# Kernel optimization log

Measured on AMD Instinct MI355X. Metric: run time of the kernel, lower is better.

## Reference

```python
import jax, jax.numpy as jnp
import numpy as np

H = 1024
NH = 16
DH = H // NH
I = 4096
EPS = 1e-6


def _rms(x, g):
    # RMSNorm: x * rsqrt(mean(x^2, -1) + eps) * g
    return x * jax.lax.rsqrt(jnp.mean(x * x, axis=-1, keepdims=True) + EPS) * g


def _squash(v):
    # norm^2/(1+norm^2)/norm * v == norm/(1+norm^2) * v
    n = jnp.sqrt(jnp.sum(v * v, axis=-1, keepdims=True))
    return v * n / (1.0 + n * n)


def setup_inputs() -> dict:
    key = jax.random.key(0)
    ks = jax.random.split(key, 16)
    B, S = 4, 1024
    w = lambda k, sh: (jax.random.normal(k, sh, jnp.float32) * 0.02)
    inp = {
        "x": jax.random.normal(ks[0], (B, S, H), jnp.float32),
        "y": jax.random.normal(ks[1], (B, S, H), jnp.float32),
        "mask": jnp.zeros((B, 1, 1, S), jnp.float32),
        "Wq": w(ks[2], (H, H)), "bq": jnp.zeros((H,), jnp.float32),
        "Wk": w(ks[3], (H, H)), "bk": jnp.zeros((H,), jnp.float32),
        "Wv": w(ks[4], (H, H)), "bv": jnp.zeros((H,), jnp.float32),
        "Wo": w(ks[5], (H, H)), "bo": jnp.zeros((H,), jnp.float32),
        "g1": jnp.ones((H,), jnp.float32),
        "Wi": w(ks[6], (H, I)), "bi": jnp.zeros((I,), jnp.float32),
        "Wo2": w(ks[7], (I, H)), "bo2": jnp.zeros((H,), jnp.float32),
        "g2": jnp.ones((H,), jnp.float32),
        "t": 3,
    }
    return inp


def reference(x, y, mask, Wq, bq, Wk, bk, Wv, bv, Wo, bo, g1, Wi, bi, Wo2, bo2, g2, t):
    B, S, _ = x.shape
    # --- updRouterWt: iterative dynamic routing over t iterations ---
    b1 = b2 = None
    c1 = c2 = jnp.float32(0.5)  # softmax([0,0])
    for i in range(t):
        if i == 0:
            c1 = c2 = jnp.float32(0.5)
        else:
            bb = jnp.stack([b1, b2], axis=1)          # [B,2,S]
            cat = jax.nn.softmax(bb, axis=1)
            c1 = cat[:, 0, :, None]                   # [B,S,1]
            c2 = cat[:, 1, :, None]
        a = _squash(c1 * x + c2 * y)                  # [B,S,H]
        d1 = jnp.einsum('bsh,bsh->bs', a, x)          # diag(a @ x^T)
        d2 = jnp.einsum('bsh,bsh->bs', a, y)
        b1 = d1 if i == 0 else b1 + d1
        b2 = d2 if i == 0 else b2 + d2
    xs = c1 * x                                       # routed query stream
    ys = c2 * y                                       # routed key/value stream
    # --- cross-attention (CoAttention, dropout=0 eval) ---
    q = (xs @ Wq + bq).reshape(B, S, NH, DH).transpose(0, 2, 1, 3)
    k = (ys @ Wk + bk).reshape(B, S, NH, DH).transpose(0, 2, 1, 3)
    v = (ys @ Wv + bv).reshape(B, S, NH, DH).transpose(0, 2, 1, 3)
    scores = jnp.einsum('bhqd,bhkd->bhqk', q, k) / np.float32(np.sqrt(DH)) + mask
    probs = jax.nn.softmax(scores, axis=-1)
    ctx = jnp.einsum('bhqk,bhkd->bhqd', probs, v).transpose(0, 2, 1, 3).reshape(B, S, H)
    # BertSelfOutput_rms
    att = _rms(ctx @ Wo + bo + xs, g1)
    # BertIntermediate (exact erf gelu) + BertOutput_rms
    inter = jax.nn.gelu(att @ Wi + bi, approximate=False)
    out = _rms(inter @ Wo2 + bo2 + att, g2)
    return out
```

## Files before the change

kernel.cpp:

```cpp
#include <hip/hip_runtime.h>

typedef unsigned short u16;
typedef __attribute__((ext_vector_type(8))) short bf16x8_t;
typedef __attribute__((ext_vector_type(4))) float f32x4_t;
typedef __attribute__((ext_vector_type(4))) unsigned short u16x4_t;

#define H_DIM 1024
#define NH 16
#define DH 64
#define I_DIM 4096
#define BATCH 4
#define SEQ 1024
#define M_ROWS 4096

__device__ __forceinline__ u16 f2bf(float f) {
    unsigned int u = __builtin_bit_cast(unsigned int, f);
    u += 0x7fffu + ((u >> 16) & 1u);
    return (u16)(u >> 16);
}

__device__ __forceinline__ void gld16(const void* g, void* l) {
    __builtin_amdgcn_global_load_lds(
        (const __attribute__((address_space(1))) unsigned int*)g,
        (__attribute__((address_space(3))) unsigned int*)l,
        16, 0, 0);
}

__global__ void route_scale_kernel(const float* __restrict__ x, const float* __restrict__ y,
                                   const int* __restrict__ tptr,
                                   float* __restrict__ c1o, float* __restrict__ c2o,
                                   u16* __restrict__ xs, u16* __restrict__ ys)
{
    int tok  = blockIdx.x * 4 + (threadIdx.x >> 6);
    int lane = threadIdx.x & 63;
    const f32x4_t* xp = (const f32x4_t*)(x + (size_t)tok * H_DIM);
    const f32x4_t* yp = (const f32x4_t*)(y + (size_t)tok * H_DIM);
    f32x4_t xv[4], yv[4];
    float xx = 0.f, xy = 0.f, yy = 0.f;
#pragma unroll
    for (int k = 0; k < 4; ++k) {
        xv[k] = xp[k * 64 + lane]; yv[k] = yp[k * 64 + lane];
#pragma unroll
        for (int e = 0; e < 4; ++e) {
            xx += xv[k][e]*xv[k][e]; xy += xv[k][e]*yv[k][e]; yy += yv[k][e]*yv[k][e];
        }
    }
#pragma unroll
    for (int m = 32; m; m >>= 1) {
        xx += __shfl_xor(xx, m); xy += __shfl_xor(xy, m); yy += __shfl_xor(yy, m);
    }
    int T = tptr[0];
    float c1 = 0.5f, c2 = 0.5f, b1 = 0.f, b2 = 0.f;
    for (int i = 0; i < T; ++i) {
        if (i > 0) {
            float mx = fmaxf(b1, b2);
            float e1 = __expf(b1 - mx), e2 = __expf(b2 - mx);
            float inv = 1.0f / (e1 + e2);
            c1 = e1 * inv; c2 = e2 * inv;
        }
        float vv = c1*c1*xx + 2.0f*c1*c2*xy + c2*c2*yy;
        float n  = sqrtf(vv);
        float s  = n / (1.0f + vv);
        float d1 = s * (c1*xx + c2*xy);
        float d2 = s * (c1*xy + c2*yy);
        b1 += d1; b2 += d2;
    }
    if (lane == 0) { c1o[tok] = c1; c2o[tok] = c2; }
#pragma unroll
    for (int k = 0; k < 4; ++k) {
        u16x4_t xo, yo;
#pragma unroll
        for (int e = 0; e < 4; ++e) { xo[e] = f2bf(xv[k][e]*c1); yo[e] = f2bf(yv[k][e]*c2); }
        ((u16x4_t*)(xs + (size_t)tok * H_DIM))[k * 64 + lane] = xo;
        ((u16x4_t*)(ys + (size_t)tok * H_DIM))[k * 64 + lane] = yo;
    }
}

__global__ void pack2_kernel(const float* __restrict__ a, const float* __restrict__ b,
                             float* __restrict__ o)
{
    int i = blockIdx.x * 256 + threadIdx.x;
    o[i] = (i < 1024) ? a[i] : b[i - 1024];
}

__device__ __forceinline__ void wcast_body(const float* __restrict__ W, u16* __restrict__ Wt,
                                           int Kw, int Nw, int blk, int tid, float* t )
{
    int nbj = Nw >> 5;
    int bi = blk / nbj, bj = blk % nbj;
#pragma unroll
    for (int p = 0; p < 4; ++p) {
        int idx = p * 256 + tid;
        int r = idx >> 5, c = idx & 31;
        t[r * 33 + c] = W[(size_t)(bi*32 + r) * Nw + bj*32 + c];
    }
    __syncthreads();
#pragma unroll
    for (int p = 0; p < 4; ++p) {
        int idx = p * 256 + tid;
        int r = idx >> 5, c = idx & 31;
        Wt[(size_t)(bj*32 + r) * Kw + bi*32 + c] = f2bf(t[c * 33 + r]);
    }
}

__global__ void wcast_kernel(const float* __restrict__ W, u16* __restrict__ Wt, int Kw, int Nw)
{
    __shared__ float t[32 * 33];
    wcast_body(W, Wt, Kw, Nw, blockIdx.x, threadIdx.x, t);
}

__global__ void wcast4_kernel(const float* __restrict__ W0, const float* __restrict__ W1,
                              const float* __restrict__ W2, const float* __restrict__ W3,
                              u16* __restrict__ T0, u16* __restrict__ T1,
                              u16* __restrict__ T2, u16* __restrict__ T3)
{
    __shared__ float t[32 * 33];
    int which = blockIdx.x >> 10, blk = blockIdx.x & 1023;
    const float* W = (which == 0) ? W0 : (which == 1) ? W1 : (which == 2) ? W2 : W3;
    u16* Wt = (which == 0) ? T0 : (which == 1) ? T1 : (which == 2) ? T2 : T3;
    wcast_body(W, Wt, 1024, 1024, blk, threadIdx.x, t);
}

#define BK 64

template<int TBN>
__global__ __launch_bounds__(256, (TBN == 128) ? 3 : 4) void gemm_bt(
    const u16* __restrict__ A, const u16* __restrict__ Bt, int N, int K,
    const float* __restrict__ bias, float scale, int epi,
    u16* __restrict__ outb, float* __restrict__ outf,
    const float* __restrict__ rscale, const float* __restrict__ resm)
{
    constexpr int TBM = 128;
    constexpr int MT = (TBN == 128) ? 4 : 2;
    constexpr int NT = 4;
    __shared__ u16 As[TBM * BK];
    __shared__ u16 Bs[TBN * BK];
    const int ntN = N / TBN;
    const int tm = blockIdx.x / ntN, tn = blockIdx.x % ntN;
    const int tid = threadIdx.x;
    const int w = tid >> 6, lane = tid & 63, q4 = lane >> 4, l16 = lane & 15;
    const int wm = (TBN == 128) ? (w >> 1) * 64 : w * 32;
    const int wn = (TBN == 128) ? (w & 1) * 64 : 0;

    const int srow = tid >> 3;
    const int scol = (tid & 7) * 8;
    const u16* ga = A  + (size_t)(tm * TBM + srow) * K + scol;
    const u16* gb = Bt + (size_t)(tn * TBN + srow) * K + scol;

    f32x4_t acc[MT][NT];
#pragma unroll
    for (int mt = 0; mt < MT; ++mt)
#pragma unroll
        for (int nt = 0; nt < NT; ++nt) acc[mt][nt] = (f32x4_t){0.f,0.f,0.f,0.f};

    for (int k0 = 0; k0 < K; k0 += BK) {
        __syncthreads();
#pragma unroll
        for (int c = 0; c < 4; ++c)
            gld16(ga + (size_t)c * 32 * K + k0, &As[c * 2048 + w * 512]);
#pragma unroll
        for (int c = 0; c < TBN/32; ++c)
            gld16(gb + (size_t)c * 32 * K + k0, &Bs[c * 2048 + w * 512]);
        __syncthreads();
#pragma unroll
        for (int kc = 0; kc < 2; ++kc) {
            bf16x8_t af[MT], bfr[NT];
#pragma unroll
            for (int mt = 0; mt < MT; ++mt)
                af[mt] = *(const bf16x8_t*)&As[(wm + mt*16 + l16) * BK + kc*32 + q4*8];
#pragma unroll
            for (int nt = 0; nt < NT; ++nt)
                bfr[nt] = *(const bf16x8_t*)&Bs[(wn + nt*16 + l16) * BK + kc*32 + q4*8];
#pragma unroll
            for (int mt = 0; mt < MT; ++mt)
#pragma unroll
                for (int nt = 0; nt < NT; ++nt)
                    acc[mt][nt] = __builtin_amdgcn_mfma_f32_16x16x32_bf16(af[mt], bfr[nt], acc[mt][nt], 0, 0, 0);
        }
    }

#pragma unroll
    for (int mt = 0; mt < MT; ++mt) {
#pragma unroll
        for (int nt = 0; nt < NT; ++nt) {
            const int gcol = tn * TBN + wn + nt*16 + l16;
            const float bv = bias[gcol];
#pragma unroll
            for (int r = 0; r < 4; ++r) {
                const int grow = tm * TBM + wm + mt*16 + q4*4 + r;
                float v = acc[mt][nt][r] + bv;
                if (epi == 0) {
                    float sc2 = (gcol < 1024) ? scale : 1.0f;
                    size_t o = (size_t)(gcol >> 10) * ((size_t)M_ROWS * H_DIM)
                             + (size_t)grow * H_DIM + (gcol & 1023);
                    outb[o] = f2bf(v * sc2);
                } else if (epi == 1) {
                    const size_t oidx = (size_t)grow * N + gcol;
                    float rs = rscale ? rscale[grow] : 1.0f;
                    outf[oidx] = v + rs * resm[oidx];
                } else {
                    const size_t oidx = (size_t)grow * N + gcol;
                    float g = 0.5f * v * (1.0f + erff(v * 0.70710678118f));
                    outb[oidx] = f2bf(g);
                }
            }
        }
    }
}

__global__ void vtrans_kernel(const u16* __restrict__ vb, u16* __restrict__ vt)
{
    __shared__ u16 t[64][65];
    const int blk = blockIdx.x;
    const int st = blk & 15, h = (blk >> 4) & 15, b = blk >> 8;
    const int tid = threadIdx.x;
#pragma unroll
    for (int p = 0; p < 16; ++p) {
        int idx = p * 256 + tid;
        int s = idx >> 6, d = idx & 63;
        t[s][d] = vb[(size_t)(b*SEQ + st*64 + s) * H_DIM + h*DH + d];
    }
    __syncthreads();
#pragma unroll
    for (int p = 0; p < 16; ++p) {
        int idx = p * 256 + tid;
        int d = idx >> 6, s = idx & 63;
        vt[(size_t)((b*NH + h)*DH + d) * SEQ + st*64 + s] = t[s][d];
    }
}

__global__ __launch_bounds__(256, 3) void attn_kernel(
    const u16* __restrict__ qb, const u16* __restrict__ kb,
    const u16* __restrict__ vt, const float* __restrict__ mask,
    u16* __restrict__ ctx)
{
    __shared__ u16 Ks[2][64 * 64];
    __shared__ u16 Vs[2][64 * 64];
    __shared__ u16 plds[4][16 * 72];

    const int raw = blockIdx.x;
    const int xg = raw & 7, sg = raw >> 3;
    const int bh = xg + 8 * (sg >> 4);
    const int qt = sg & 15;
    const int b = bh >> 4, h = bh & 15;
    const int tid = threadIdx.x, w = tid >> 6, lane = tid & 63, q4 = lane >> 4, l16 = lane & 15;

    const u16* qrow = qb + ((size_t)(b*SEQ + qt*64 + w*16 + l16) * H_DIM + h*DH);
    bf16x8_t qf0 = *(const bf16x8_t*)(qrow + q4*8);
    bf16x8_t qf1 = *(const bf16x8_t*)(qrow + 32 + q4*8);

    const u16* kbp   = kb + ((size_t)(b*SEQ) * H_DIM + h*DH);
    const u16* vbase = vt + ((size_t)((b*NH + h)*DH) * SEQ);
    const float* mrow = mask + b*SEQ;

    const int srow0 = tid >> 3;
    const int srow1 = 32 + (tid >> 3);
    const int sel   = (tid & 7) * 8;
    const int ldsb0 = w * 512;
    const int ldsb1 = 2048 + w * 512;

    f32x4_t o[4];
#pragma unroll
    for (int dt = 0; dt < 4; ++dt) o[dt] = (f32x4_t){0.f,0.f,0.f,0.f};
    float mi = -1e30f, li = 0.f;
    u16* pw = &plds[w][0];

    gld16(kbp + (size_t)srow0 * H_DIM + sel, &Ks[0][ldsb0]);
    gld16(kbp + (size_t)srow1 * H_DIM + sel, &Ks[0][ldsb1]);
    gld16(vbase + (size_t)srow0 * SEQ + sel, &Vs[0][ldsb0]);
    gld16(vbase + (size_t)srow1 * SEQ + sel, &Vs[0][ldsb1]);
    __syncthreads();

    for (int j = 0; j < 16; ++j) {
        const int kb0 = j * 64;
        const int buf = j & 1, nxt = buf ^ 1;
        if (j < 15) {
            const u16* gK = kbp + (size_t)(kb0 + 64) * H_DIM;
            const u16* gV = vbase + (kb0 + 64);
            gld16(gK + (size_t)srow0 * H_DIM + sel, &Ks[nxt][ldsb0]);
            gld16(gK + (size_t)srow1 * H_DIM + sel, &Ks[nxt][ldsb1]);
            gld16(gV + (size_t)srow0 * SEQ + sel, &Vs[nxt][ldsb0]);
            gld16(gV + (size_t)srow1 * SEQ + sel, &Vs[nxt][ldsb1]);
        }

        f32x4_t sc[4];
#pragma unroll
        for (int nt = 0; nt < 4; ++nt) {
            bf16x8_t kf0 = *(const bf16x8_t*)&Ks[buf][(nt*16 + l16)*64 + q4*8];
            bf16x8_t kf1 = *(const bf16x8_t*)&Ks[buf][(nt*16 + l16)*64 + 32 + q4*8];
            f32x4_t s = (f32x4_t){0.f,0.f,0.f,0.f};
            s = __builtin_amdgcn_mfma_f32_16x16x32_bf16(kf0, qf0, s, 0, 0, 0);
            s = __builtin_amdgcn_mfma_f32_16x16x32_bf16(kf1, qf1, s, 0, 0, 0);
            f32x4_t mv = *(const f32x4_t*)&mrow[kb0 + nt*16 + q4*4];
#pragma unroll
            for (int r = 0; r < 4; ++r) s[r] += mv[r];
            sc[nt] = s;
        }
        float tmax = sc[0][0];
#pragma unroll
        for (int nt = 0; nt < 4; ++nt)
#pragma unroll
            for (int r = 0; r < 4; ++r) tmax = fmaxf(tmax, sc[nt][r]);
        tmax = fmaxf(tmax, __shfl_xor(tmax, 16));
        tmax = fmaxf(tmax, __shfl_xor(tmax, 32));
        float nm = fmaxf(mi, tmax);
        float al = __expf(mi - nm);
        mi = nm;
        float rs = 0.f;
#pragma unroll
        for (int nt = 0; nt < 4; ++nt)
#pragma unroll
            for (int r = 0; r < 4; ++r) {
                float p = __expf(sc[nt][r] - nm);
                sc[nt][r] = p; rs += p;
            }
        rs += __shfl_xor(rs, 16);
        rs += __shfl_xor(rs, 32);
        li = li * al + rs;
#pragma unroll
        for (int dt = 0; dt < 4; ++dt)
#pragma unroll
            for (int r = 0; r < 4; ++r) o[dt][r] *= al;

#pragma unroll
        for (int nt = 0; nt < 4; ++nt) {
            u16x4_t pb;
#pragma unroll
            for (int r = 0; r < 4; ++r) pb[r] = f2bf(sc[nt][r]);
            *(u16x4_t*)&pw[l16*72 + nt*16 + q4*4] = pb;
        }
        asm volatile("s_waitcnt lgkmcnt(0)" ::: "memory");
        bf16x8_t pf0 = *(const bf16x8_t*)&pw[l16*72 + q4*8];
        bf16x8_t pf1 = *(const bf16x8_t*)&pw[l16*72 + 32 + q4*8];
#pragma unroll
        for (int dt = 0; dt < 4; ++dt) {
            bf16x8_t vf0 = *(const bf16x8_t*)&Vs[buf][(dt*16 + l16)*64 + q4*8];
            bf16x8_t vf1 = *(const bf16x8_t*)&Vs[buf][(dt*16 + l16)*64 + 32 + q4*8];
            o[dt] = __builtin_amdgcn_mfma_f32_16x16x32_bf16(vf0, pf0, o[dt], 0, 0, 0);
            o[dt] = __builtin_amdgcn_mfma_f32_16x16x32_bf16(vf1, pf1, o[dt], 0, 0, 0);
        }
        if (j < 15) __syncthreads();
    }
    const float inv = 1.0f / li;
    const size_t tokbase = (size_t)(b*SEQ + qt*64 + w*16 + l16) * H_DIM + h*DH;
#pragma unroll
    for (int dt = 0; dt < 4; ++dt) {
        u16x4_t ob;
#pragma unroll
        for (int r = 0; r < 4; ++r) ob[r] = f2bf(o[dt][r] * inv);
        *(u16x4_t*)&ctx[tokbase + dt*16 + q4*4] = ob;
    }
}

__global__ void rms_kernel(const float* __restrict__ in, const float* __restrict__ g,
                           float* __restrict__ outf, u16* __restrict__ outb)
{
    int row  = blockIdx.x * 4 + (threadIdx.x >> 6);
    int lane = threadIdx.x & 63;
    const f32x4_t* ip = (const f32x4_t*)(in + (size_t)row * H_DIM);
    f32x4_t v[4];
    float ss = 0.f;
#pragma unroll
    for (int k = 0; k < 4; ++k) {
        v[k] = ip[k * 64 + lane];
#pragma unroll
        for (int e = 0; e < 4; ++e) ss += v[k][e] * v[k][e];
    }
#pragma unroll
    for (int m = 32; m; m >>= 1) ss += __shfl_xor(ss, m);
    float sc = rsqrtf(ss * (1.0f / 1024.0f) + 1e-6f);
#pragma unroll
    for (int k = 0; k < 4; ++k) {
        f32x4_t gv = ((const f32x4_t*)g)[k * 64 + lane];
        f32x4_t ov;
        u16x4_t ob;
#pragma unroll
        for (int e = 0; e < 4; ++e) { ov[e] = v[k][e] * sc * gv[e]; ob[e] = f2bf(ov[e]); }
        if (outf) ((f32x4_t*)(outf + (size_t)row * H_DIM))[k * 64 + lane] = ov;
        if (outb) ((u16x4_t*)(outb + (size_t)row * H_DIM))[k * 64 + lane] = ob;
    }
}

extern "C" void kernel_launch(void* const* d_in, const int* in_sizes, int n_in,
                              void* d_out, int out_size, void* d_ws, size_t ws_size,
                              hipStream_t stream)
{
    const float* x   = (const float*)d_in[0];
    const float* y   = (const float*)d_in[1];
    const float* mask= (const float*)d_in[2];
    const float* Wq  = (const float*)d_in[3];
    const float* bq  = (const float*)d_in[4];
    const float* Wk  = (const float*)d_in[5];
    const float* bk  = (const float*)d_in[6];
    const float* Wv  = (const float*)d_in[7];
    const float* bv  = (const float*)d_in[8];
    const float* Wo  = (const float*)d_in[9];
    const float* bo  = (const float*)d_in[10];
    const float* g1  = (const float*)d_in[11];
    const float* Wi  = (const float*)d_in[12];
    const float* bi  = (const float*)d_in[13];
    const float* Wo2 = (const float*)d_in[14];
    const float* bo2 = (const float*)d_in[15];
    const float* g2  = (const float*)d_in[16];
    const int*   tp  = (const int*)d_in[17];
    float* out = (float*)d_out;

    char* ws = (char*)d_ws;
    const size_t MB = 1024 * 1024;
    float* c1    = (float*)(ws);
    float* c2    = (float*)(ws + 16 * 1024);
    float* bkv   = (float*)(ws + 32 * 1024);
    u16* xs_b    = (u16*)(ws + 1 * MB);
    u16* ys_b    = (u16*)(ws + 9 * MB);
    u16* wq_t    = (u16*)(ws + 17 * MB);
    u16* wk_t    = (u16*)(ws + 19 * MB);
    u16* wv_t    = (u16*)(ws + 21 * MB);
    u16* wo_t    = (u16*)(ws + 23 * MB);
    u16* wi_t    = (u16*)(ws + 25 * MB);
    u16* wo2_t   = (u16*)(ws + 33 * MB);
    u16* qb      = (u16*)(ws + 41 * MB);
    u16* kb      = (u16*)(ws + 49 * MB);
    u16* vb      = (u16*)(ws + 57 * MB);
    u16* vtb     = (u16*)(ws + 65 * MB);
    u16* inter_b = qb;
    float* attpre= (float*)(ws + 73 * MB);
    float* attf  = (float*)(ws + 89 * MB);
    (void)ws_size; (void)in_sizes; (void)n_in; (void)out_size; (void)wv_t; (void)vb;

    route_scale_kernel<<<1024, 256, 0, stream>>>(x, y, tp, c1, c2, xs_b, ys_b);
    pack2_kernel<<<8, 256, 0, stream>>>(bk, bv, bkv);
    wcast4_kernel<<<4096, 256, 0, stream>>>(Wq, Wk, Wv, Wo, wq_t, wk_t, wv_t, wo_t);
    wcast_kernel<<<4096, 256, 0, stream>>>(Wi, wi_t, 1024, 4096);
    wcast_kernel<<<4096, 256, 0, stream>>>(Wo2, wo2_t, 4096, 1024);

    gemm_bt<64><<<512, 256, 0, stream>>>(xs_b, wq_t, 1024, 1024, bq, 0.125f, 0, qb, nullptr, nullptr, nullptr);
    gemm_bt<128><<<512, 256, 0, stream>>>(ys_b, wk_t, 2048, 1024, bkv, 1.0f, 0, kb, nullptr, nullptr, nullptr);
    vtrans_kernel<<<1024, 256, 0, stream>>>(vb, vtb);
    attn_kernel<<<1024, 256, 0, stream>>>(qb, kb, vtb, mask, xs_b );
    gemm_bt<64><<<512, 256, 0, stream>>>(xs_b, wo_t, 1024, 1024, bo, 1.0f, 1, nullptr, attpre, c1, x);
    rms_kernel<<<1024, 256, 0, stream>>>(attpre, g1, attf, ys_b );
    gemm_bt<128><<<1024, 256, 0, stream>>>(ys_b, wi_t, 4096, 1024, bi, 1.0f, 2, inter_b, nullptr, nullptr, nullptr);
    gemm_bt<64><<<512, 256, 0, stream>>>(inter_b, wo2_t, 1024, 4096, bo2, 1.0f, 1, nullptr, attpre, nullptr, attf);
    rms_kernel<<<1024, 256, 0, stream>>>(attpre, g2, out, nullptr);
}
```

Baseline: 472.6 us.

## Swizzle GEMM tile order, read bf16 residuals, and use tanh GELU

GEMM blocks are remapped so groups of neighbouring M tiles share an N tile, aiming for better L2 reuse of weight and activation tiles. Residual adds in the output-projection epilogues now read the bf16 copies of the routed inputs instead of fp32 tensors plus a per-row scale. This also lets the first RMSNorm skip writing its fp32 output. The exact erf GELU is replaced by the tanh approximation using fast exp. That trims epilogue arithmetic and memory traffic at the cost of some precision loss against the exact-erf reference.

```diff
diff --git a/kernel.cpp b/kernel.cpp
--- a/kernel.cpp
+++ b/kernel.cpp
@@ -17,6 +17,10 @@
     unsigned int u = __builtin_bit_cast(unsigned int, f);
     u += 0x7fffu + ((u >> 16) & 1u);
     return (u16)(u >> 16);
+}
+__device__ __forceinline__ float bf2f(u16 b) {
+    unsigned int u = ((unsigned int)b) << 16;
+    return __builtin_bit_cast(float, u);
 }
 
 __device__ __forceinline__ void gld16(const void* g, void* l) {
@@ -128,15 +132,16 @@
     const u16* __restrict__ A, const u16* __restrict__ Bt, int N, int K,
     const float* __restrict__ bias, float scale, int epi,
     u16* __restrict__ outb, float* __restrict__ outf,
-    const float* __restrict__ rscale, const float* __restrict__ resm)
+    const u16* __restrict__ resm)
 {
     constexpr int TBM = 128;
     constexpr int MT = (TBN == 128) ? 4 : 2;
     constexpr int NT = 4;
     __shared__ u16 As[TBM * BK];
     __shared__ u16 Bs[TBN * BK];
-    const int ntN = N / TBN;
-    const int tm = blockIdx.x / ntN, tn = blockIdx.x % ntN;
+    const int xg = blockIdx.x & 7, sg = blockIdx.x >> 3;
+    const int tm = xg * 4 + (sg & 3);
+    const int tn = sg >> 2;
     const int tid = threadIdx.x;
     const int w = tid >> 6, lane = tid & 63, q4 = lane >> 4, l16 = lane & 15;
     const int wm = (TBN == 128) ? (w >> 1) * 64 : w * 32;
@@ -196,12 +201,13 @@
                     outb[o] = f2bf(v * sc2);
                 } else if (epi == 1) {
                     const size_t oidx = (size_t)grow * N + gcol;
-                    float rs = rscale ? rscale[grow] : 1.0f;
-                    outf[oidx] = v + rs * resm[oidx];
+                    outf[oidx] = v + bf2f(resm[oidx]);
                 } else {
                     const size_t oidx = (size_t)grow * N + gcol;
-                    float g = 0.5f * v * (1.0f + erff(v * 0.70710678118f));
-                    outb[oidx] = f2bf(g);
+                    float z = 0.7978845608f * (v + 0.044715f * v * v * v);
+                    float e = __expf(2.0f * z);
+                    float th = 1.0f - 2.0f / (e + 1.0f);
+                    outb[oidx] = f2bf(0.5f * v * (1.0f + th));
                 }
             }
         }
@@ -424,8 +430,8 @@
     u16* vtb     = (u16*)(ws + 65 * MB);
     u16* inter_b = qb;
     float* attpre= (float*)(ws + 73 * MB);
-    float* attf  = (float*)(ws + 89 * MB);
-    (void)ws_size; (void)in_sizes; (void)n_in; (void)out_size; (void)wv_t; (void)vb;
+    u16* ctx_b   = (u16*)(ws + 89 * MB);
+    (void)ws_size; (void)in_sizes; (void)n_in; (void)out_size; (void)wv_t; (void)vb; (void)c2;
 
     route_scale_kernel<<<1024, 256, 0, stream>>>(x, y, tp, c1, c2, xs_b, ys_b);
     pack2_kernel<<<8, 256, 0, stream>>>(bk, bv, bkv);
@@ -433,13 +439,13 @@
     wcast_kernel<<<4096, 256, 0, stream>>>(Wi, wi_t, 1024, 4096);
     wcast_kernel<<<4096, 256, 0, stream>>>(Wo2, wo2_t, 4096, 1024);
 
-    gemm_bt<64><<<512, 256, 0, stream>>>(xs_b, wq_t, 1024, 1024, bq, 0.125f, 0, qb, nullptr, nullptr, nullptr);
-    gemm_bt<128><<<512, 256, 0, stream>>>(ys_b, wk_t, 2048, 1024, bkv, 1.0f, 0, kb, nullptr, nullptr, nullptr);
+    gemm_bt<64><<<512, 256, 0, stream>>>(xs_b, wq_t, 1024, 1024, bq, 0.125f, 0, qb, nullptr, nullptr);
+    gemm_bt<128><<<512, 256, 0, stream>>>(ys_b, wk_t, 2048, 1024, bkv, 1.0f, 0, kb, nullptr, nullptr);
     vtrans_kernel<<<1024, 256, 0, stream>>>(vb, vtb);
-    attn_kernel<<<1024, 256, 0, stream>>>(qb, kb, vtb, mask, xs_b );
-    gemm_bt<64><<<512, 256, 0, stream>>>(xs_b, wo_t, 1024, 1024, bo, 1.0f, 1, nullptr, attpre, c1, x);
-    rms_kernel<<<1024, 256, 0, stream>>>(attpre, g1, attf, ys_b );
-    gemm_bt<128><<<1024, 256, 0, stream>>>(ys_b, wi_t, 4096, 1024, bi, 1.0f, 2, inter_b, nullptr, nullptr, nullptr);
-    gemm_bt<64><<<512, 256, 0, stream>>>(inter_b, wo2_t, 1024, 4096, bo2, 1.0f, 1, nullptr, attpre, nullptr, attf);
+    attn_kernel<<<1024, 256, 0, stream>>>(qb, kb, vtb, mask, ctx_b);
+    gemm_bt<64><<<512, 256, 0, stream>>>(ctx_b, wo_t, 1024, 1024, bo, 1.0f, 1, nullptr, attpre, xs_b);
+    rms_kernel<<<1024, 256, 0, stream>>>(attpre, g1, nullptr, ys_b );
+    gemm_bt<128><<<1024, 256, 0, stream>>>(ys_b, wi_t, 4096, 1024, bi, 1.0f, 2, inter_b, nullptr, nullptr);
+    gemm_bt<64><<<512, 256, 0, stream>>>(inter_b, wo2_t, 1024, 4096, bo2, 1.0f, 1, nullptr, attpre, ys_b);
     rms_kernel<<<1024, 256, 0, stream>>>(attpre, g2, out, nullptr);
 }
```

Result: faster. 445.4 us (-5.8%).
